# Kernel optimization log

Hardware: AMD Instinct MI355X
Metric: run time of the kernel (lower is better)

The kernel has to match this reference:

```python
import jax, jax.numpy as jnp
import numpy as np

N_NODES = 100000
N_EDGES = 1600000
DIM = 64
NEG_SLOPE = 0.2  # DGL GATConv default
BN_EPS = 1e-5


def setup_inputs() -> dict:
    key = jax.random.key(0)
    ks = jax.random.split(key, 16)
    d = {}
    d["node_weight"] = jax.random.normal(ks[0], (N_NODES, DIM), jnp.float32)
    d["edge_weight"] = jax.random.normal(ks[1], (N_EDGES,), jnp.float32)  # unused in forward (faithful to source)
    d["src"] = jax.random.randint(ks[2], (N_EDGES,), 0, N_NODES)
    d["dst"] = jax.random.randint(ks[3], (N_EDGES,), 0, N_NODES)
    i = 4
    scale = 1.0 / np.sqrt(DIM)
    for l in (1, 2, 3):
        d[f"W{l}"] = jax.random.normal(ks[i], (DIM, DIM), jnp.float32) * scale; i += 1
        d[f"al{l}"] = jax.random.normal(ks[i], (DIM,), jnp.float32) * 0.1; i += 1
        d[f"ar{l}"] = jax.random.normal(ks[i], (DIM,), jnp.float32) * 0.1; i += 1
        d[f"b{l}"] = jnp.zeros((DIM,), jnp.float32)
        d[f"g{l}"] = jnp.ones((DIM,), jnp.float32)
        d[f"beta{l}"] = jnp.zeros((DIM,), jnp.float32)
    return d


def gat_layer(h, src, dst, W, al, ar, b):
    # DGL GATConv, 1 head: project, edge attention, per-dst softmax, scatter-add
    feat = h @ W                                  # [N, D]
    el = feat @ al                                # [N]
    er = feat @ ar                                # [N]
    e = jax.nn.leaky_relu(el[src] + er[dst], NEG_SLOPE)   # [E]
    m = jax.ops.segment_max(e, dst, num_segments=N_NODES)  # per-dst max
    ex = jnp.exp(e - m[dst])
    s = jax.ops.segment_sum(ex, dst, num_segments=N_NODES)
    alpha = ex / s[dst]                           # edge softmax
    out = jax.ops.segment_sum(alpha[:, None] * feat[src], dst, num_segments=N_NODES)
    return out + b


def batchnorm(h, g, beta):
    # BatchNorm1d in training mode: batch stats, biased variance
    mu = jnp.mean(h, axis=0)
    var = jnp.mean(jnp.square(h - mu), axis=0)
    return (h - mu) * jax.lax.rsqrt(var + BN_EPS) * g + beta


def reference(node_weight, edge_weight, src, dst,
              W1, al1, ar1, b1, g1, beta1,
              W2, al2, ar2, b2, g2, beta2,
              W3, al3, ar3, b3, g3, beta3):
    # dropout is identity in eval mode
    h = gat_layer(node_weight, src, dst, W1, al1, ar1, b1)
    h = jax.nn.elu(batchnorm(h, g1, beta1))
    h = gat_layer(h, src, dst, W2, al2, ar2, b2)
    h = jax.nn.elu(batchnorm(h, g2, beta2))
    h = gat_layer(h, src, dst, W3, al3, ar3, b3)
    h = batchnorm(h, g3, beta3)
    return h
```

## Files before the change

kernel.cpp:

```cpp
#include <hip/hip_runtime.h>
#include <hip/hip_bf16.h>
#include <math.h>

#define DIM 64
#define BSHIFT 9
#define BNODES 512
#define MAXB 256
#define EPT 8
#define CHUNK 2048

typedef __attribute__((ext_vector_type(8))) short bf16x8;
typedef __attribute__((ext_vector_type(4))) float f32x4;

__device__ __forceinline__ short f2bf(float x) {
    union { __hip_bfloat16 b; short s; } u;
    u.b = __float2bfloat16(x);
    return u.s;
}
__device__ __forceinline__ float bf2f(short s) {
    return __uint_as_float(((unsigned)(unsigned short)s) << 16);
}


__global__ void bin_count_kernel(const int* __restrict__ dst, int* __restrict__ bucket_cnt, int E) {
    __shared__ int h[MAXB];
    int t = threadIdx.x;
    h[t] = 0;
    __syncthreads();
    for (int i = blockIdx.x * blockDim.x + t; i < E; i += gridDim.x * blockDim.x)
        atomicAdd(&h[dst[i] >> BSHIFT], 1);
    __syncthreads();
    if (h[t]) atomicAdd(&bucket_cnt[t], h[t]);
}

__global__ void bucket_scan_kernel(const int* __restrict__ bucket_cnt,
                                   int* __restrict__ bucket_off, int* __restrict__ bucket_fill) {
    __shared__ int s[MAXB];
    int t = threadIdx.x;
    int v = bucket_cnt[t];
    s[t] = v;
    __syncthreads();
    for (int off = 1; off < MAXB; off <<= 1) {
        int x = (t >= off) ? s[t - off] : 0;
        __syncthreads();
        s[t] += x;
        __syncthreads();
    }
    bucket_off[t] = s[t] - v;
    bucket_fill[t] = 0;
}

__global__ __launch_bounds__(256) void bin_scatter_kernel(
    const int* __restrict__ src, const int* __restrict__ dst,
    const int* __restrict__ bucket_off, int* __restrict__ bucket_fill,
    unsigned long long* __restrict__ binned, int E) {
    __shared__ int lcnt[MAXB];
    __shared__ int lbase[MAXB];
    int t = threadIdx.x;
    lcnt[t] = 0;
    __syncthreads();
    int base = blockIdx.x * CHUNK;
    unsigned long long pair[EPT];
    int slot[EPT];
#pragma unroll
    for (int j = 0; j < EPT; j++) {
        int idx = base + j * 256 + t;
        if (idx < E) {
            int s = src[idx], d = dst[idx];
            pair[j] = ((unsigned long long)(unsigned)d << 32) | (unsigned)s;
            slot[j] = atomicAdd(&lcnt[d >> BSHIFT], 1);
        } else {
            slot[j] = -1;
        }
    }
    __syncthreads();
    int c = lcnt[t];
    if (c) lbase[t] = atomicAdd(&bucket_fill[t], c);
    __syncthreads();
#pragma unroll
    for (int j = 0; j < EPT; j++) {
        if (slot[j] >= 0) {
            int b = (int)(pair[j] >> 32) >> BSHIFT;
            binned[(size_t)bucket_off[b] + lbase[b] + slot[j]] = pair[j];
        }
    }
}

__global__ __launch_bounds__(256) void node_count_kernel(
    const unsigned long long* __restrict__ binned, const int* __restrict__ bucket_off,
    const int* __restrict__ bucket_cnt, int* __restrict__ counts, int N) {
    __shared__ int cnt[BNODES];
    int b = blockIdx.x, t = threadIdx.x;
    for (int i = t; i < BNODES; i += 256) cnt[i] = 0;
    __syncthreads();
    int s0 = bucket_off[b], c = bucket_cnt[b];
    for (int i = t; i < c; i += 256) {
        int d = (int)(binned[(size_t)s0 + i] >> 32);
        atomicAdd(&cnt[d & (BNODES - 1)], 1);
    }
    __syncthreads();
    int nbase = b << BSHIFT;
    for (int i = t; i < BNODES; i += 256)
        if (nbase + i < N) counts[nbase + i] = cnt[i];
}

__global__ void scan1_kernel(const int* __restrict__ counts, int* __restrict__ excl,
                             int* __restrict__ blk_sums, int n) {
    __shared__ int sdata[256];
    int t = threadIdx.x;
    int base = blockIdx.x * 1024 + t * 4;
    int v0 = (base + 0 < n) ? counts[base + 0] : 0;
    int v1 = (base + 1 < n) ? counts[base + 1] : 0;
    int v2 = (base + 2 < n) ? counts[base + 2] : 0;
    int v3 = (base + 3 < n) ? counts[base + 3] : 0;
    int tsum = v0 + v1 + v2 + v3;
    sdata[t] = tsum;
    __syncthreads();
    for (int off = 1; off < 256; off <<= 1) {
        int x = (t >= off) ? sdata[t - off] : 0;
        __syncthreads();
        sdata[t] += x;
        __syncthreads();
    }
    int run = sdata[t] - tsum;
    if (base + 0 < n) excl[base + 0] = run; run += v0;
    if (base + 1 < n) excl[base + 1] = run; run += v1;
    if (base + 2 < n) excl[base + 2] = run; run += v2;
    if (base + 3 < n) excl[base + 3] = run;
    if (t == 255) blk_sums[blockIdx.x] = sdata[255];
}

__global__ void scan2_kernel(int* __restrict__ blk_sums, int nb) {
    __shared__ int s[128];
    int t = threadIdx.x;
    s[t] = (t < nb) ? blk_sums[t] : 0;
    __syncthreads();
    for (int off = 1; off < 128; off <<= 1) {
        int x = (t >= off) ? s[t - off] : 0;
        __syncthreads();
        s[t] += x;
        __syncthreads();
    }
    if (t < nb) blk_sums[t] = (t > 0) ? s[t - 1] : 0;
}

__global__ void scan3_kernel(int* __restrict__ excl, const int* __restrict__ blk_sums,
                             int n, int total) {
    int i = blockIdx.x * blockDim.x + threadIdx.x;
    if (i < n) excl[i] += blk_sums[i >> 10];
    if (i == 0) excl[n] = total;
}

__global__ __launch_bounds__(256) void final_scatter_kernel(
    const unsigned long long* __restrict__ binned, const int* __restrict__ bucket_off,
    const int* __restrict__ bucket_cnt, const int* __restrict__ row_ptr,
    int* __restrict__ src_sorted, int N) {
    __shared__ int fill[BNODES];
    int b = blockIdx.x, t = threadIdx.x;
    for (int i = t; i < BNODES; i += 256) fill[i] = 0;
    __syncthreads();
    int s0 = bucket_off[b], c = bucket_cnt[b];
    for (int i = t; i < c; i += 256) {
        unsigned long long p = binned[(size_t)s0 + i];
        int d = (int)(p >> 32);
        int pos = row_ptr[d] + atomicAdd(&fill[d & (BNODES - 1)], 1);
        src_sorted[pos] = (int)(p & 0xffffffffu);
    }
}


__global__ __launch_bounds__(256) void gemm64_mfma_kernel(
    const float* __restrict__ h, const float* __restrict__ W,
    const float* __restrict__ al, const float* __restrict__ ar,
    const float* __restrict__ stats, const float* __restrict__ g,
    const float* __restrict__ beta, int do_bn, float invN,
    __hip_bfloat16* __restrict__ feat, float* __restrict__ el, float* __restrict__ er,
    int n) {
    int t = threadIdx.x;
    int lane = t & 63;
    int li = lane & 15;
    int quad = lane >> 4;
    int wv = t >> 6;

    bf16x8 b_hi[2][4], b_lo[2][4];
#pragma unroll
    for (int ks = 0; ks < 2; ks++)
#pragma unroll
        for (int nt = 0; nt < 4; nt++) {
#pragma unroll
            for (int j = 0; j < 8; j++) {
                float w = W[(ks * 32 + quad * 8 + j) * 64 + nt * 16 + li];
                short hi = f2bf(w);
                b_hi[ks][nt][j] = hi;
                b_lo[ks][nt][j] = f2bf(w - bf2f(hi));
            }
        }
    float alv[4], arv[4];
#pragma unroll
    for (int nt = 0; nt < 4; nt++) { alv[nt] = al[nt * 16 + li]; arv[nt] = ar[nt * 16 + li]; }

    float sc[2][8], sh[2][8];
    if (do_bn) {
#pragma unroll
        for (int ks = 0; ks < 2; ks++)
#pragma unroll
            for (int j = 0; j < 8; j++) {
                int k = ks * 32 + quad * 8 + j;
                float mu = stats[k] * invN;
                float var = fmaf(-mu, mu, stats[64 + k] * invN);
                float inv = rsqrtf(var + 1e-5f) * g[k];
                sc[ks][j] = inv;
                sh[ks][j] = beta[k] - mu * inv;
            }
    }

    int ntiles = (n + 15) >> 4;
    for (int tile = blockIdx.x * 4 + wv; tile < ntiles; tile += gridDim.x * 4) {
        int m0 = tile << 4;
        int rrow = m0 + li;
        const float* rowp = h + (size_t)((rrow < n) ? rrow : (n - 1)) * 64;
        bf16x8 a_hi[2], a_lo[2];
#pragma unroll
        for (int ks = 0; ks < 2; ks++) {
            float4 v0 = *(const float4*)(rowp + ks * 32 + quad * 8);
            float4 v1 = *(const float4*)(rowp + ks * 32 + quad * 8 + 4);
            float x[8] = {v0.x, v0.y, v0.z, v0.w, v1.x, v1.y, v1.z, v1.w};
#pragma unroll
            for (int j = 0; j < 8; j++) {
                float v = x[j];
                if (do_bn) {
                    v = fmaf(v, sc[ks][j], sh[ks][j]);
                    if (v < 0.f) v = expm1f(v);
                }
                short hi = f2bf(v);
                a_hi[ks][j] = hi;
                a_lo[ks][j] = f2bf(v - bf2f(hi));
            }
        }
        f32x4 acc[4];
#pragma unroll
        for (int nt = 0; nt < 4; nt++) acc[nt] = (f32x4){0.f, 0.f, 0.f, 0.f};
#pragma unroll
        for (int ks = 0; ks < 2; ks++)
#pragma unroll
            for (int nt = 0; nt < 4; nt++) {
                acc[nt] = __builtin_amdgcn_mfma_f32_16x16x32_bf16(a_hi[ks], b_hi[ks][nt], acc[nt], 0, 0, 0);
                acc[nt] = __builtin_amdgcn_mfma_f32_16x16x32_bf16(a_lo[ks], b_hi[ks][nt], acc[nt], 0, 0, 0);
                acc[nt] = __builtin_amdgcn_mfma_f32_16x16x32_bf16(a_hi[ks], b_lo[ks][nt], acc[nt], 0, 0, 0);
            }
#pragma unroll
        for (int nt = 0; nt < 4; nt++)
#pragma unroll
            for (int reg = 0; reg < 4; reg++) {
                int wrow = m0 + quad * 4 + reg;
                if (wrow < n) {
                    union { __hip_bfloat16 b; short s; } u;
                    u.s = f2bf(acc[nt][reg]);
                    feat[(size_t)wrow * 64 + nt * 16 + li] = u.b;
                }
            }
        float pl[4], pr[4];
#pragma unroll
        for (int reg = 0; reg < 4; reg++) {
            float l = 0.f, r = 0.f;
#pragma unroll
            for (int nt = 0; nt < 4; nt++) {
                l = fmaf(acc[nt][reg], alv[nt], l);
                r = fmaf(acc[nt][reg], arv[nt], r);
            }
#pragma unroll
            for (int off = 1; off < 16; off <<= 1) {
                l += __shfl_xor(l, off, 64);
                r += __shfl_xor(r, off, 64);
            }
            pl[reg] = l; pr[reg] = r;
        }
        int row = m0 + quad * 4;
        if (li == 0 && row < n)          { el[row] = pl[0]; er[row] = pr[0]; }
        else if (li == 1 && row + 1 < n) { el[row + 1] = pl[1]; er[row + 1] = pr[1]; }
        else if (li == 2 && row + 2 < n) { el[row + 2] = pl[2]; er[row + 2] = pr[2]; }
        else if (li == 3 && row + 3 < n) { el[row + 3] = pl[3]; er[row + 3] = pr[3]; }
    }
}

__global__ __launch_bounds__(256) void attn_kernel(
    const int* __restrict__ row_ptr, const int* __restrict__ src_sorted,
    const float* __restrict__ el, const float* __restrict__ er,
    float* __restrict__ ebuf, int n) {
    int t = threadIdx.x;
    int li = t & 15;
    int node = blockIdx.x * 16 + (t >> 4);
    if (node >= n) return;
    int start = row_ptr[node], end = row_ptr[node + 1];
    float er_n = er[node];

    float m = -INFINITY, s = 0.f;
    for (int i = start + li; i < end; i += 16) {
        float v = el[src_sorted[i]] + er_n;
        v = (v > 0.f) ? v : 0.2f * v;
        ebuf[i] = v;
        float mn = fmaxf(m, v);
        s = s * __expf(m - mn) + __expf(v - mn);
        m = mn;
    }
#pragma unroll
    for (int off = 8; off; off >>= 1) {
        float mo = __shfl_xor(m, off, 64);
        float so = __shfl_xor(s, off, 64);
        float mn = fmaxf(m, mo);
        float sa = (m == -INFINITY) ? 0.f : s * __expf(m - mn);
        float sb = (mo == -INFINITY) ? 0.f : so * __expf(mo - mn);
        s = sa + sb;
        m = mn;
    }
    float inv_s = (s > 0.f) ? 1.f / s : 0.f;
    for (int i = start + li; i < end; i += 16) {
        ebuf[i] = __expf(ebuf[i] - m) * inv_s;
    }
}

__global__ __launch_bounds__(256) void aggregate_kernel(
    const int* __restrict__ row_ptr, const int* __restrict__ src_sorted,
    const float* __restrict__ alpha, const __hip_bfloat16* __restrict__ feat,
    const float* __restrict__ bias, float* __restrict__ out, int n) {
    int t = threadIdx.x, lane = t & 63;
    int q = lane >> 3;
    int li = lane & 7;
    int node = blockIdx.x * 4 + (t >> 6);
    if (node >= n) return;
    int start = row_ptr[node], end = row_ptr[node + 1];
    const uint4* featv = (const uint4*)feat;

    float a0 = 0.f, a1 = 0.f, a2 = 0.f, a3 = 0.f, a4 = 0.f, a5 = 0.f, a6 = 0.f, a7 = 0.f;
    int i = start;
    for (; i + 8 <= end; i += 8) {
        int idx = i + q;
        float a = alpha[idx];
        int sn = src_sorted[idx];
        uint4 p = featv[(size_t)sn * 8 + li];
        a0 = fmaf(a, __uint_as_float(p.x << 16), a0);
        a1 = fmaf(a, __uint_as_float(p.x & 0xffff0000u), a1);
        a2 = fmaf(a, __uint_as_float(p.y << 16), a2);
        a3 = fmaf(a, __uint_as_float(p.y & 0xffff0000u), a3);
        a4 = fmaf(a, __uint_as_float(p.z << 16), a4);
        a5 = fmaf(a, __uint_as_float(p.z & 0xffff0000u), a5);
        a6 = fmaf(a, __uint_as_float(p.w << 16), a6);
        a7 = fmaf(a, __uint_as_float(p.w & 0xffff0000u), a7);
    }
    if (i < end) {
        int idx = i + q;
        bool valid = idx < end;
        int idc = valid ? idx : end - 1;
        float a = valid ? alpha[idc] : 0.f;
        int sn = src_sorted[idc];
        uint4 p = featv[(size_t)sn * 8 + li];
        a0 = fmaf(a, __uint_as_float(p.x << 16), a0);
        a1 = fmaf(a, __uint_as_float(p.x & 0xffff0000u), a1);
        a2 = fmaf(a, __uint_as_float(p.y << 16), a2);
        a3 = fmaf(a, __uint_as_float(p.y & 0xffff0000u), a3);
        a4 = fmaf(a, __uint_as_float(p.z << 16), a4);
        a5 = fmaf(a, __uint_as_float(p.z & 0xffff0000u), a5);
        a6 = fmaf(a, __uint_as_float(p.w << 16), a6);
        a7 = fmaf(a, __uint_as_float(p.w & 0xffff0000u), a7);
    }
#pragma unroll
    for (int off = 8; off <= 32; off <<= 1) {
        a0 += __shfl_xor(a0, off, 64);
        a1 += __shfl_xor(a1, off, 64);
        a2 += __shfl_xor(a2, off, 64);
        a3 += __shfl_xor(a3, off, 64);
        a4 += __shfl_xor(a4, off, 64);
        a5 += __shfl_xor(a5, off, 64);
        a6 += __shfl_xor(a6, off, 64);
        a7 += __shfl_xor(a7, off, 64);
    }
    if (q == 0) {
        const float4* bv = (const float4*)bias;
        float4 b0 = bv[li * 2], b1 = bv[li * 2 + 1];
        float4 o0 = {a0 + b0.x, a1 + b0.y, a2 + b0.z, a3 + b0.w};
        float4 o1 = {a4 + b1.x, a5 + b1.y, a6 + b1.z, a7 + b1.w};
        float4* op = (float4*)(out + (size_t)node * 64 + li * 8);
        op[0] = o0;
        op[1] = o1;
    }
}

__global__ __launch_bounds__(256) void bn_stats_kernel(const float* __restrict__ h,
                                                       float* __restrict__ stats, int n) {
    __shared__ float ls[256], lss[256];
    int t = threadIdx.x, lane = t & 63;
    int w = blockIdx.x * 4 + (t >> 6);
    int stride = gridDim.x * 4;
    float s = 0.f, ss = 0.f;
    for (int row = w; row < n; row += stride) {
        float v = h[(size_t)row * DIM + lane];
        s += v;
        ss = fmaf(v, v, ss);
    }
    ls[t] = s; lss[t] = ss;
    __syncthreads();
    if (t < 64) {
        float a = ls[t] + ls[t + 64] + ls[t + 128] + ls[t + 192];
        float b = lss[t] + lss[t + 64] + lss[t + 128] + lss[t + 192];
        atomicAdd(&stats[t], a);
        atomicAdd(&stats[64 + t], b);
    }
}

__global__ void bn_apply_kernel(float* __restrict__ h, const float* __restrict__ stats,
                                const float* __restrict__ g, const float* __restrict__ beta,
                                int n, int do_elu) {
    int i = blockIdx.x * blockDim.x + threadIdx.x;
    int total = n * DIM;
    int stride = gridDim.x * blockDim.x;
    float invN = 1.f / (float)n;
    for (; i < total; i += stride) {
        int c = i & 63;
        float mu = stats[c] * invN;
        float var = fmaf(-mu, mu, stats[DIM + c] * invN);
        float x = (h[i] - mu) * rsqrtf(var + 1e-5f) * g[c] + beta[c];
        if (do_elu && x < 0.f) x = expm1f(x);
        h[i] = x;
    }
}


extern "C" void kernel_launch(void* const* d_in, const int* in_sizes, int n_in,
                              void* d_out, int out_size, void* d_ws, size_t ws_size,
                              hipStream_t stream) {
    const float* nw = (const float*)d_in[0];
    const int* src = (const int*)d_in[2];
    const int* dst = (const int*)d_in[3];
    const int N = in_sizes[0] / DIM;
    const int E = in_sizes[2];
    const float invN = 1.f / (float)N;
    const int nbuck = (N + BNODES - 1) >> BSHIFT;

    char* ws = (char*)d_ws;
    size_t off = 0;
    auto alloc = [&](size_t bytes) -> void* {
        void* p = ws + off;
        off += (bytes + 255) & ~(size_t)255;
        return p;
    };
    int* counts       = (int*)alloc((size_t)N * 4);
    int* row_ptr      = (int*)alloc(((size_t)N + 1) * 4);
    int* blk_sums     = (int*)alloc(512);
    int* bucket_cnt   = (int*)alloc(MAXB * 4);
    int* bucket_off   = (int*)alloc(MAXB * 4);
    int* bucket_fill  = (int*)alloc(MAXB * 4);
    unsigned long long* binned = (unsigned long long*)alloc((size_t)E * 8);
    int* src_sorted   = (int*)alloc((size_t)E * 4);
    float* ebuf       = (float*)alloc((size_t)E * 4);
    float* el         = (float*)alloc((size_t)N * 4);
    float* er         = (float*)alloc((size_t)N * 4);
    __hip_bfloat16* feat = (__hip_bfloat16*)alloc((size_t)N * DIM * 2);
    float* hbuf       = (float*)alloc((size_t)N * DIM * 4);
    float* stats      = (float*)alloc(512);

    int nb = (N + 1023) / 1024;

    hipMemsetAsync(bucket_cnt, 0, MAXB * 4, stream);
    bin_count_kernel<<<256, 256, 0, stream>>>(dst, bucket_cnt, E);
    bucket_scan_kernel<<<1, MAXB, 0, stream>>>(bucket_cnt, bucket_off, bucket_fill);
    bin_scatter_kernel<<<(E + CHUNK - 1) / CHUNK, 256, 0, stream>>>(
        src, dst, bucket_off, bucket_fill, binned, E);
    node_count_kernel<<<nbuck, 256, 0, stream>>>(binned, bucket_off, bucket_cnt, counts, N);
    scan1_kernel<<<nb, 256, 0, stream>>>(counts, row_ptr, blk_sums, N);
    scan2_kernel<<<1, 128, 0, stream>>>(blk_sums, nb);
    scan3_kernel<<<(N + 255) / 256, 256, 0, stream>>>(row_ptr, blk_sums, N, E);
    final_scatter_kernel<<<nbuck, 256, 0, stream>>>(binned, bucket_off, bucket_cnt,
                                                    row_ptr, src_sorted, N);

    for (int l = 0; l < 3; l++) {
        const float* W    = (const float*)d_in[4 + 6 * l];
        const float* al   = (const float*)d_in[5 + 6 * l];
        const float* ar   = (const float*)d_in[6 + 6 * l];
        const float* b    = (const float*)d_in[7 + 6 * l];
        const float* g    = (const float*)d_in[8 + 6 * l];
        const float* beta = (const float*)d_in[9 + 6 * l];
        const float* hin = (l == 0) ? nw : hbuf;
        float* hout = (l == 2) ? (float*)d_out : hbuf;

        gemm64_mfma_kernel<<<1024, 256, 0, stream>>>(
            hin, W, al, ar, stats,
            (l == 0) ? al : (const float*)d_in[8 + 6 * (l - 1)],
            (l == 0) ? al : (const float*)d_in[9 + 6 * (l - 1)],
            (l > 0) ? 1 : 0, invN,
            feat, el, er, N);
        attn_kernel<<<(N + 15) / 16, 256, 0, stream>>>(row_ptr, src_sorted, el, er, ebuf, N);
        aggregate_kernel<<<(N + 3) / 4, 256, 0, stream>>>(row_ptr, src_sorted, ebuf,
                                                          feat, b, hout, N);
        hipMemsetAsync(stats, 0, 512, stream);
        bn_stats_kernel<<<512, 256, 0, stream>>>(hout, stats, N);
    }
    bn_apply_kernel<<<2048, 256, 0, stream>>>((float*)d_out, stats,
                                              (const float*)d_in[8 + 12],
                                              (const float*)d_in[9 + 12],
                                              N, 0);
}
```

Before: 515.4 us.

## Fuse edge softmax into aggregation with online softmax and recomputed el

```diff
diff --git a/kernel.cpp b/kernel.cpp
--- a/kernel.cpp
+++ b/kernel.cpp
@@ -171,10 +171,10 @@
 
 __global__ __launch_bounds__(256) void gemm64_mfma_kernel(
     const float* __restrict__ h, const float* __restrict__ W,
-    const float* __restrict__ al, const float* __restrict__ ar,
+    const float* __restrict__ ar,
     const float* __restrict__ stats, const float* __restrict__ g,
     const float* __restrict__ beta, int do_bn, float invN,
-    __hip_bfloat16* __restrict__ feat, float* __restrict__ el, float* __restrict__ er,
+    __hip_bfloat16* __restrict__ feat, float* __restrict__ er,
     int n) {
     int t = threadIdx.x;
     int lane = t & 63;
@@ -195,9 +195,9 @@
                 b_lo[ks][nt][j] = f2bf(w - bf2f(hi));
             }
         }
-    float alv[4], arv[4];
-#pragma unroll
-    for (int nt = 0; nt < 4; nt++) { alv[nt] = al[nt * 16 + li]; arv[nt] = ar[nt * 16 + li]; }
+    float arv[4];
+#pragma unroll
+    for (int nt = 0; nt < 4; nt++) arv[nt] = ar[nt * 16 + li];
 
     float sc[2][8], sh[2][8];
     if (do_bn) {
@@ -259,109 +259,114 @@
                     feat[(size_t)wrow * 64 + nt * 16 + li] = u.b;
                 }
             }
-        float pl[4], pr[4];
+        float pr[4];
 #pragma unroll
         for (int reg = 0; reg < 4; reg++) {
-            float l = 0.f, r = 0.f;
-#pragma unroll
-            for (int nt = 0; nt < 4; nt++) {
-                l = fmaf(acc[nt][reg], alv[nt], l);
+            float r = 0.f;
+#pragma unroll
+            for (int nt = 0; nt < 4; nt++)
                 r = fmaf(acc[nt][reg], arv[nt], r);
-            }
-#pragma unroll
-            for (int off = 1; off < 16; off <<= 1) {
-                l += __shfl_xor(l, off, 64);
+#pragma unroll
+            for (int off = 1; off < 16; off <<= 1)
                 r += __shfl_xor(r, off, 64);
-            }
-            pl[reg] = l; pr[reg] = r;
+            pr[reg] = r;
         }
         int row = m0 + quad * 4;
-        if (li == 0 && row < n)          { el[row] = pl[0]; er[row] = pr[0]; }
-        else if (li == 1 && row + 1 < n) { el[row + 1] = pl[1]; er[row + 1] = pr[1]; }
-        else if (li == 2 && row + 2 < n) { el[row + 2] = pl[2]; er[row + 2] = pr[2]; }
-        else if (li == 3 && row + 3 < n) { el[row + 3] = pl[3]; er[row + 3] = pr[3]; }
-    }
-}
-
-__global__ __launch_bounds__(256) void attn_kernel(
+        if (li == 0 && row < n)          er[row] = pr[0];
+        else if (li == 1 && row + 1 < n) er[row + 1] = pr[1];
+        else if (li == 2 && row + 2 < n) er[row + 2] = pr[2];
+        else if (li == 3 && row + 3 < n) er[row + 3] = pr[3];
+    }
+}
+
+__global__ __launch_bounds__(256) void attn_agg_kernel(
     const int* __restrict__ row_ptr, const int* __restrict__ src_sorted,
-    const float* __restrict__ el, const float* __restrict__ er,
-    float* __restrict__ ebuf, int n) {
-    int t = threadIdx.x;
-    int li = t & 15;
-    int node = blockIdx.x * 16 + (t >> 4);
-    if (node >= n) return;
-    int start = row_ptr[node], end = row_ptr[node + 1];
-    float er_n = er[node];
-
-    float m = -INFINITY, s = 0.f;
-    for (int i = start + li; i < end; i += 16) {
-        float v = el[src_sorted[i]] + er_n;
-        v = (v > 0.f) ? v : 0.2f * v;
-        ebuf[i] = v;
-        float mn = fmaxf(m, v);
-        s = s * __expf(m - mn) + __expf(v - mn);
-        m = mn;
-    }
-#pragma unroll
-    for (int off = 8; off; off >>= 1) {
-        float mo = __shfl_xor(m, off, 64);
-        float so = __shfl_xor(s, off, 64);
-        float mn = fmaxf(m, mo);
-        float sa = (m == -INFINITY) ? 0.f : s * __expf(m - mn);
-        float sb = (mo == -INFINITY) ? 0.f : so * __expf(mo - mn);
-        s = sa + sb;
-        m = mn;
-    }
-    float inv_s = (s > 0.f) ? 1.f / s : 0.f;
-    for (int i = start + li; i < end; i += 16) {
-        ebuf[i] = __expf(ebuf[i] - m) * inv_s;
-    }
-}
-
-__global__ __launch_bounds__(256) void aggregate_kernel(
-    const int* __restrict__ row_ptr, const int* __restrict__ src_sorted,
-    const float* __restrict__ alpha, const __hip_bfloat16* __restrict__ feat,
-    const float* __restrict__ bias, float* __restrict__ out, int n) {
+    const float* __restrict__ er, const __hip_bfloat16* __restrict__ feat,
+    const float* __restrict__ al, const float* __restrict__ bias,
+    float* __restrict__ out, int n) {
     int t = threadIdx.x, lane = t & 63;
     int q = lane >> 3;
     int li = lane & 7;
     int node = blockIdx.x * 4 + (t >> 6);
     if (node >= n) return;
     int start = row_ptr[node], end = row_ptr[node + 1];
+    float er_n = er[node];
+    const float4* al4 = (const float4*)al;
+    float4 A0 = al4[li * 2], A1 = al4[li * 2 + 1];
     const uint4* featv = (const uint4*)feat;
 
+    float m = -INFINITY, s = 0.f;
     float a0 = 0.f, a1 = 0.f, a2 = 0.f, a3 = 0.f, a4 = 0.f, a5 = 0.f, a6 = 0.f, a7 = 0.f;
+
     int i = start;
-    for (; i + 8 <= end; i += 8) {
-        int idx = i + q;
-        float a = alpha[idx];
-        int sn = src_sorted[idx];
-        uint4 p = featv[(size_t)sn * 8 + li];
-        a0 = fmaf(a, __uint_as_float(p.x << 16), a0);
-        a1 = fmaf(a, __uint_as_float(p.x & 0xffff0000u), a1);
-        a2 = fmaf(a, __uint_as_float(p.y << 16), a2);
-        a3 = fmaf(a, __uint_as_float(p.y & 0xffff0000u), a3);
-        a4 = fmaf(a, __uint_as_float(p.z << 16), a4);
-        a5 = fmaf(a, __uint_as_float(p.z & 0xffff0000u), a5);
-        a6 = fmaf(a, __uint_as_float(p.w << 16), a6);
-        a7 = fmaf(a, __uint_as_float(p.w & 0xffff0000u), a7);
-    }
+    bool v0 = false;
+    uint4 p0 = {0u, 0u, 0u, 0u};
     if (i < end) {
         int idx = i + q;
-        bool valid = idx < end;
-        int idc = valid ? idx : end - 1;
-        float a = valid ? alpha[idc] : 0.f;
+        v0 = idx < end;
+        int idc = v0 ? idx : end - 1;
         int sn = src_sorted[idc];
-        uint4 p = featv[(size_t)sn * 8 + li];
-        a0 = fmaf(a, __uint_as_float(p.x << 16), a0);
-        a1 = fmaf(a, __uint_as_float(p.x & 0xffff0000u), a1);
-        a2 = fmaf(a, __uint_as_float(p.y << 16), a2);
-        a3 = fmaf(a, __uint_as_float(p.y & 0xffff0000u), a3);
-        a4 = fmaf(a, __uint_as_float(p.z << 16), a4);
-        a5 = fmaf(a, __uint_as_float(p.z & 0xffff0000u), a5);
-        a6 = fmaf(a, __uint_as_float(p.w << 16), a6);
-        a7 = fmaf(a, __uint_as_float(p.w & 0xffff0000u), a7);
+        p0 = featv[(size_t)sn * 8 + li];
+    }
+    while (i < end) {
+        int inext = i + 8;
+        bool v1 = false;
+        uint4 p1 = {0u, 0u, 0u, 0u};
+        if (inext < end) {
+            int idx = inext + q;
+            v1 = idx < end;
+            int idc = v1 ? idx : end - 1;
+            int sn = src_sorted[idc];
+            p1 = featv[(size_t)sn * 8 + li];
+        }
+        float f0 = __uint_as_float(p0.x << 16);
+        float f1 = __uint_as_float(p0.x & 0xffff0000u);
+        float f2 = __uint_as_float(p0.y << 16);
+        float f3 = __uint_as_float(p0.y & 0xffff0000u);
+        float f4 = __uint_as_float(p0.z << 16);
+        float f5 = __uint_as_float(p0.z & 0xffff0000u);
+        float f6 = __uint_as_float(p0.w << 16);
+        float f7 = __uint_as_float(p0.w & 0xffff0000u);
+        float d = f0 * A0.x;
+        d = fmaf(f1, A0.y, d);
+        d = fmaf(f2, A0.z, d);
+        d = fmaf(f3, A0.w, d);
+        d = fmaf(f4, A1.x, d);
+        d = fmaf(f5, A1.y, d);
+        d = fmaf(f6, A1.z, d);
+        d = fmaf(f7, A1.w, d);
+        d += __shfl_xor(d, 1, 64);
+        d += __shfl_xor(d, 2, 64);
+        d += __shfl_xor(d, 4, 64);
+        float e = d + er_n;
+        e = (e > 0.f) ? e : 0.2f * e;
+        if (!v0) e = -INFINITY;
+        float em = e;
+        em = fmaxf(em, __shfl_xor(em, 8, 64));
+        em = fmaxf(em, __shfl_xor(em, 16, 64));
+        em = fmaxf(em, __shfl_xor(em, 32, 64));
+        if (em > m) {
+            float r = __expf(m - em);
+            s *= r;
+            a0 *= r; a1 *= r; a2 *= r; a3 *= r;
+            a4 *= r; a5 *= r; a6 *= r; a7 *= r;
+            m = em;
+        }
+        float w = __expf(e - m);
+        float ws = w;
+        ws += __shfl_xor(ws, 8, 64);
+        ws += __shfl_xor(ws, 16, 64);
+        ws += __shfl_xor(ws, 32, 64);
+        s += ws;
+        a0 = fmaf(w, f0, a0);
+        a1 = fmaf(w, f1, a1);
+        a2 = fmaf(w, f2, a2);
+        a3 = fmaf(w, f3, a3);
+        a4 = fmaf(w, f4, a4);
+        a5 = fmaf(w, f5, a5);
+        a6 = fmaf(w, f6, a6);
+        a7 = fmaf(w, f7, a7);
+        i = inext; v0 = v1; p0 = p1;
     }
 #pragma unroll
     for (int off = 8; off <= 32; off <<= 1) {
@@ -374,11 +379,14 @@
         a6 += __shfl_xor(a6, off, 64);
         a7 += __shfl_xor(a7, off, 64);
     }
+    float inv_s = (s > 0.f) ? 1.f / s : 0.f;
     if (q == 0) {
         const float4* bv = (const float4*)bias;
         float4 b0 = bv[li * 2], b1 = bv[li * 2 + 1];
-        float4 o0 = {a0 + b0.x, a1 + b0.y, a2 + b0.z, a3 + b0.w};
-        float4 o1 = {a4 + b1.x, a5 + b1.y, a6 + b1.z, a7 + b1.w};
+        float4 o0 = {fmaf(a0, inv_s, b0.x), fmaf(a1, inv_s, b0.y),
+                     fmaf(a2, inv_s, b0.z), fmaf(a3, inv_s, b0.w)};
+        float4 o1 = {fmaf(a4, inv_s, b1.x), fmaf(a5, inv_s, b1.y),
+                     fmaf(a6, inv_s, b1.z), fmaf(a7, inv_s, b1.w)};
         float4* op = (float4*)(out + (size_t)node * 64 + li * 8);
         op[0] = o0;
         op[1] = o1;
@@ -451,8 +459,6 @@
     int* bucket_fill  = (int*)alloc(MAXB * 4);
     unsigned long long* binned = (unsigned long long*)alloc((size_t)E * 8);
     int* src_sorted   = (int*)alloc((size_t)E * 4);
-    float* ebuf       = (float*)alloc((size_t)E * 4);
-    float* el         = (float*)alloc((size_t)N * 4);
     float* er         = (float*)alloc((size_t)N * 4);
     __hip_bfloat16* feat = (__hip_bfloat16*)alloc((size_t)N * DIM * 2);
     float* hbuf       = (float*)alloc((size_t)N * DIM * 4);
@@ -483,14 +489,13 @@
         float* hout = (l == 2) ? (float*)d_out : hbuf;
 
         gemm64_mfma_kernel<<<1024, 256, 0, stream>>>(
-            hin, W, al, ar, stats,
-            (l == 0) ? al : (const float*)d_in[8 + 6 * (l - 1)],
-            (l == 0) ? al : (const float*)d_in[9 + 6 * (l - 1)],
+            hin, W, ar, stats,
+            (l == 0) ? ar : (const float*)d_in[8 + 6 * (l - 1)],
+            (l == 0) ? ar : (const float*)d_in[9 + 6 * (l - 1)],
             (l > 0) ? 1 : 0, invN,
-            feat, el, er, N);
-        attn_kernel<<<(N + 15) / 16, 256, 0, stream>>>(row_ptr, src_sorted, el, er, ebuf, N);
-        aggregate_kernel<<<(N + 3) / 4, 256, 0, stream>>>(row_ptr, src_sorted, ebuf,
-                                                          feat, b, hout, N);
+            feat, er, N);
+        attn_agg_kernel<<<(N + 3) / 4, 256, 0, stream>>>(row_ptr, src_sorted, er,
+                                                         feat, al, b, hout, N);
         hipMemsetAsync(stats, 0, 512, stream);
         bn_stats_kernel<<<512, 256, 0, stream>>>(hout, stats, N);
     }
```

Result: no change. 505.5 us (-1.9%).

## Fuse edge softmax into aggregation and prefetch next edge batch

Applied to the files above, without the earlier changes.

```diff
diff --git a/kernel.cpp b/kernel.cpp
--- a/kernel.cpp
+++ b/kernel.cpp
@@ -283,88 +283,65 @@
     }
 }
 
-__global__ __launch_bounds__(256) void attn_kernel(
+__global__ __launch_bounds__(256) void attn_agg_kernel(
     const int* __restrict__ row_ptr, const int* __restrict__ src_sorted,
     const float* __restrict__ el, const float* __restrict__ er,
-    float* __restrict__ ebuf, int n) {
-    int t = threadIdx.x;
-    int li = t & 15;
-    int node = blockIdx.x * 16 + (t >> 4);
-    if (node >= n) return;
-    int start = row_ptr[node], end = row_ptr[node + 1];
-    float er_n = er[node];
-
-    float m = -INFINITY, s = 0.f;
-    for (int i = start + li; i < end; i += 16) {
-        float v = el[src_sorted[i]] + er_n;
-        v = (v > 0.f) ? v : 0.2f * v;
-        ebuf[i] = v;
-        float mn = fmaxf(m, v);
-        s = s * __expf(m - mn) + __expf(v - mn);
-        m = mn;
-    }
-#pragma unroll
-    for (int off = 8; off; off >>= 1) {
-        float mo = __shfl_xor(m, off, 64);
-        float so = __shfl_xor(s, off, 64);
-        float mn = fmaxf(m, mo);
-        float sa = (m == -INFINITY) ? 0.f : s * __expf(m - mn);
-        float sb = (mo == -INFINITY) ? 0.f : so * __expf(mo - mn);
-        s = sa + sb;
-        m = mn;
-    }
-    float inv_s = (s > 0.f) ? 1.f / s : 0.f;
-    for (int i = start + li; i < end; i += 16) {
-        ebuf[i] = __expf(ebuf[i] - m) * inv_s;
-    }
-}
-
-__global__ __launch_bounds__(256) void aggregate_kernel(
-    const int* __restrict__ row_ptr, const int* __restrict__ src_sorted,
-    const float* __restrict__ alpha, const __hip_bfloat16* __restrict__ feat,
-    const float* __restrict__ bias, float* __restrict__ out, int n) {
+    const __hip_bfloat16* __restrict__ feat, const float* __restrict__ bias,
+    float* __restrict__ out, int n) {
     int t = threadIdx.x, lane = t & 63;
     int q = lane >> 3;
     int li = lane & 7;
     int node = blockIdx.x * 4 + (t >> 6);
     if (node >= n) return;
     int start = row_ptr[node], end = row_ptr[node + 1];
+    float er_n = er[node];
     const uint4* featv = (const uint4*)feat;
 
+    float s = 0.f;
     float a0 = 0.f, a1 = 0.f, a2 = 0.f, a3 = 0.f, a4 = 0.f, a5 = 0.f, a6 = 0.f, a7 = 0.f;
+
     int i = start;
-    for (; i + 8 <= end; i += 8) {
-        int idx = i + q;
-        float a = alpha[idx];
-        int sn = src_sorted[idx];
-        uint4 p = featv[(size_t)sn * 8 + li];
-        a0 = fmaf(a, __uint_as_float(p.x << 16), a0);
-        a1 = fmaf(a, __uint_as_float(p.x & 0xffff0000u), a1);
-        a2 = fmaf(a, __uint_as_float(p.y << 16), a2);
-        a3 = fmaf(a, __uint_as_float(p.y & 0xffff0000u), a3);
-        a4 = fmaf(a, __uint_as_float(p.z << 16), a4);
-        a5 = fmaf(a, __uint_as_float(p.z & 0xffff0000u), a5);
-        a6 = fmaf(a, __uint_as_float(p.w << 16), a6);
-        a7 = fmaf(a, __uint_as_float(p.w & 0xffff0000u), a7);
-    }
+    bool v0 = false;
+    uint4 p0 = {0u, 0u, 0u, 0u};
+    float el0 = 0.f;
     if (i < end) {
         int idx = i + q;
-        bool valid = idx < end;
-        int idc = valid ? idx : end - 1;
-        float a = valid ? alpha[idc] : 0.f;
+        v0 = idx < end;
+        int idc = v0 ? idx : end - 1;
         int sn = src_sorted[idc];
-        uint4 p = featv[(size_t)sn * 8 + li];
-        a0 = fmaf(a, __uint_as_float(p.x << 16), a0);
-        a1 = fmaf(a, __uint_as_float(p.x & 0xffff0000u), a1);
-        a2 = fmaf(a, __uint_as_float(p.y << 16), a2);
-        a3 = fmaf(a, __uint_as_float(p.y & 0xffff0000u), a3);
-        a4 = fmaf(a, __uint_as_float(p.z << 16), a4);
-        a5 = fmaf(a, __uint_as_float(p.z & 0xffff0000u), a5);
-        a6 = fmaf(a, __uint_as_float(p.w << 16), a6);
-        a7 = fmaf(a, __uint_as_float(p.w & 0xffff0000u), a7);
+        el0 = el[sn];
+        p0 = featv[(size_t)sn * 8 + li];
+    }
+    while (i < end) {
+        int inext = i + 8;
+        bool v1 = false;
+        uint4 p1 = {0u, 0u, 0u, 0u};
+        float el1 = 0.f;
+        if (inext < end) {
+            int idx = inext + q;
+            v1 = idx < end;
+            int idc = v1 ? idx : end - 1;
+            int sn = src_sorted[idc];
+            el1 = el[sn];
+            p1 = featv[(size_t)sn * 8 + li];
+        }
+        float e = el0 + er_n;
+        e = (e > 0.f) ? e : 0.2f * e;
+        float w = v0 ? __expf(e) : 0.f;
+        s += w;
+        a0 = fmaf(w, __uint_as_float(p0.x << 16), a0);
+        a1 = fmaf(w, __uint_as_float(p0.x & 0xffff0000u), a1);
+        a2 = fmaf(w, __uint_as_float(p0.y << 16), a2);
+        a3 = fmaf(w, __uint_as_float(p0.y & 0xffff0000u), a3);
+        a4 = fmaf(w, __uint_as_float(p0.z << 16), a4);
+        a5 = fmaf(w, __uint_as_float(p0.z & 0xffff0000u), a5);
+        a6 = fmaf(w, __uint_as_float(p0.w << 16), a6);
+        a7 = fmaf(w, __uint_as_float(p0.w & 0xffff0000u), a7);
+        i = inext; v0 = v1; p0 = p1; el0 = el1;
     }
 #pragma unroll
     for (int off = 8; off <= 32; off <<= 1) {
+        s  += __shfl_xor(s,  off, 64);
         a0 += __shfl_xor(a0, off, 64);
         a1 += __shfl_xor(a1, off, 64);
         a2 += __shfl_xor(a2, off, 64);
@@ -374,11 +351,14 @@
         a6 += __shfl_xor(a6, off, 64);
         a7 += __shfl_xor(a7, off, 64);
     }
+    float inv_s = (s > 0.f) ? 1.f / s : 0.f;
     if (q == 0) {
         const float4* bv = (const float4*)bias;
         float4 b0 = bv[li * 2], b1 = bv[li * 2 + 1];
-        float4 o0 = {a0 + b0.x, a1 + b0.y, a2 + b0.z, a3 + b0.w};
-        float4 o1 = {a4 + b1.x, a5 + b1.y, a6 + b1.z, a7 + b1.w};
+        float4 o0 = {fmaf(a0, inv_s, b0.x), fmaf(a1, inv_s, b0.y),
+                     fmaf(a2, inv_s, b0.z), fmaf(a3, inv_s, b0.w)};
+        float4 o1 = {fmaf(a4, inv_s, b1.x), fmaf(a5, inv_s, b1.y),
+                     fmaf(a6, inv_s, b1.z), fmaf(a7, inv_s, b1.w)};
         float4* op = (float4*)(out + (size_t)node * 64 + li * 8);
         op[0] = o0;
         op[1] = o1;
@@ -451,16 +431,16 @@
     int* bucket_fill  = (int*)alloc(MAXB * 4);
     unsigned long long* binned = (unsigned long long*)alloc((size_t)E * 8);
     int* src_sorted   = (int*)alloc((size_t)E * 4);
-    float* ebuf       = (float*)alloc((size_t)E * 4);
     float* el         = (float*)alloc((size_t)N * 4);
     float* er         = (float*)alloc((size_t)N * 4);
     __hip_bfloat16* feat = (__hip_bfloat16*)alloc((size_t)N * DIM * 2);
     float* hbuf       = (float*)alloc((size_t)N * DIM * 4);
-    float* stats      = (float*)alloc(512);
+    float* stats      = (float*)alloc(3 * 512);
 
     int nb = (N + 1023) / 1024;
 
     hipMemsetAsync(bucket_cnt, 0, MAXB * 4, stream);
+    hipMemsetAsync(stats, 0, 3 * 512, stream);
     bin_count_kernel<<<256, 256, 0, stream>>>(dst, bucket_cnt, E);
     bucket_scan_kernel<<<1, MAXB, 0, stream>>>(bucket_cnt, bucket_off, bucket_fill);
     bin_scatter_kernel<<<(E + CHUNK - 1) / CHUNK, 256, 0, stream>>>(
@@ -481,20 +461,20 @@
         const float* beta = (const float*)d_in[9 + 6 * l];
         const float* hin = (l == 0) ? nw : hbuf;
         float* hout = (l == 2) ? (float*)d_out : hbuf;
+        float* stats_prev = stats + (l - 1) * 128;
+        float* stats_cur  = stats + l * 128;
 
         gemm64_mfma_kernel<<<1024, 256, 0, stream>>>(
-            hin, W, al, ar, stats,
+            hin, W, al, ar, stats_prev,
             (l == 0) ? al : (const float*)d_in[8 + 6 * (l - 1)],
             (l == 0) ? al : (const float*)d_in[9 + 6 * (l - 1)],
             (l > 0) ? 1 : 0, invN,
             feat, el, er, N);
-        attn_kernel<<<(N + 15) / 16, 256, 0, stream>>>(row_ptr, src_sorted, el, er, ebuf, N);
-        aggregate_kernel<<<(N + 3) / 4, 256, 0, stream>>>(row_ptr, src_sorted, ebuf,
-                                                          feat, b, hout, N);
-        hipMemsetAsync(stats, 0, 512, stream);
-        bn_stats_kernel<<<512, 256, 0, stream>>>(hout, stats, N);
-    }
-    bn_apply_kernel<<<2048, 256, 0, stream>>>((float*)d_out, stats,
+        attn_agg_kernel<<<(N + 3) / 4, 256, 0, stream>>>(row_ptr, src_sorted, el, er,
+                                                         feat, b, hout, N);
+        bn_stats_kernel<<<512, 256, 0, stream>>>(hout, stats_cur, N);
+    }
+    bn_apply_kernel<<<2048, 256, 0, stream>>>((float*)d_out, stats + 2 * 128,
                                               (const float*)d_in[8 + 12],
                                               (const float*)d_in[9 + 12],
                                               N, 0);
```

Result: faster. 469.4 us (-8.9%).
